# Performance work log

Hardware: AMD Instinct MI355X
Metric: run time of the kernel (lower is better)

## Reference

```python
import jax, jax.numpy as jnp
import numpy as np

BATCH, NSTEPS, IN_F, OUT_F = 8192, 16, 256, 512


def setup_inputs() -> dict:
    key = jax.random.key(0)
    ks = jax.random.split(key, 20)
    r = jax.random.normal
    return {
        "x": r(ks[0], (BATCH, NSTEPS, IN_F), jnp.float32),
        "C": r(ks[1], (BATCH, OUT_F, 1), jnp.float32),
        "H": r(ks[2], (BATCH, OUT_F, 1), jnp.float32),
        "fg_w_c": r(ks[3], (OUT_F, 1), jnp.float32),
        "fg_w_h": r(ks[4], (OUT_F, OUT_F), jnp.float32),
        "fg_w_x": r(ks[5], (OUT_F, IN_F), jnp.float32),
        "fg_b": r(ks[6], (OUT_F, 1), jnp.float32),
        "ig_w_c": r(ks[7], (OUT_F, 1), jnp.float32),
        "ig_w_h": r(ks[8], (OUT_F, OUT_F), jnp.float32),
        "ig_w_x": r(ks[9], (OUT_F, IN_F), jnp.float32),
        "ig_b": r(ks[10], (OUT_F, 1), jnp.float32),
        "in_w_h": r(ks[11], (OUT_F, OUT_F), jnp.float32),
        "in_w_x": r(ks[12], (OUT_F, IN_F), jnp.float32),
        "in_b": r(ks[13], (OUT_F, 1), jnp.float32),
        "og_w_cn": r(ks[14], (OUT_F, 1), jnp.float32),
        "og_w_h": r(ks[15], (OUT_F, OUT_F), jnp.float32),
        "og_w_x": r(ks[16], (OUT_F, IN_F), jnp.float32),
        "og_b": r(ks[17], (OUT_F, 1), jnp.float32),
        "n": 3,
    }


def reference(x, C, H,
              fg_w_c, fg_w_h, fg_w_x, fg_b,
              ig_w_c, ig_w_h, ig_w_x, ig_b,
              in_w_h, in_w_x, in_b,
              og_w_cn, og_w_h, og_w_x, og_b,
              n):
    # x: [B, T, IN] -> current step [B, IN, 1]
    x_cur = x[:, n, :, None]
    # peephole LSTM gates; matmul broadcasts [O,O] @ [B,O,1] -> [B,O,1]
    fg = jax.nn.sigmoid(fg_w_c * C + jnp.matmul(fg_w_h, H) + jnp.matmul(fg_w_x, x_cur) + fg_b)
    ig = jax.nn.sigmoid(ig_w_c * C + jnp.matmul(ig_w_h, H) + jnp.matmul(ig_w_x, x_cur) + ig_b)
    inn = jnp.tanh(jnp.matmul(in_w_h, H) + jnp.matmul(in_w_x, x_cur) + in_b)
    cm = fg * C + ig * inn
    og = jax.nn.sigmoid(og_w_cn * cm + jnp.matmul(og_w_h, H) + jnp.matmul(og_w_x, x_cur) + og_b)
    h = og * jnp.tanh(cm)
    return (cm, h)
```

## Files before the change

kernel.cpp:

```cpp
#include <hip/hip_runtime.h>


typedef _Float16 half8 __attribute__((ext_vector_type(8)));
typedef _Float16 half4v __attribute__((ext_vector_type(4)));
typedef float floatx4 __attribute__((ext_vector_type(4)));

#define BATCH 8192
#define NSTEPS 16
#define IN_F 256
#define OUT_F 512
#define KDIM 768
#define NDIM 2048
#define HSIZE ((size_t)BATCH * OUT_F)

#define BM 128
#define BN 128
#define BK 64

__device__ __forceinline__ void async_copy16(const void* gptr, void* lptr) {
  __builtin_amdgcn_global_load_lds(
      (const __attribute__((address_space(1))) unsigned int*)gptr,
      (__attribute__((address_space(3))) unsigned int*)lptr,
      16, 0, 0);
}

__device__ __forceinline__ float sigmoidf_(float x) {
  return 1.0f / (1.0f + __expf(-x));
}

__device__ __forceinline__ float tanhf_(float x) {
  x = fminf(fmaxf(x, -20.0f), 20.0f);
  float e = __expf(2.0f * x);
  return (e - 1.0f) / (e + 1.0f);
}

__global__ void pack_A(const float* __restrict__ H, const float* __restrict__ x,
                       const int* __restrict__ nptr, _Float16* __restrict__ A) {
  const int n = *nptr;
  const int b = blockIdx.x;
  const int k = threadIdx.x * 4;
  float4 v;
  if (k < OUT_F)
    v = *(const float4*)(H + (size_t)b * OUT_F + k);
  else
    v = *(const float4*)(x + ((size_t)b * NSTEPS + n) * IN_F + (k - OUT_F));
  half4v h = {(_Float16)v.x, (_Float16)v.y, (_Float16)v.z, (_Float16)v.w};
  *(half4v*)(A + (size_t)b * KDIM + k) = h;
}

__global__ void pack_W(const float* __restrict__ fg_w_h, const float* __restrict__ fg_w_x,
                       const float* __restrict__ ig_w_h, const float* __restrict__ ig_w_x,
                       const float* __restrict__ in_w_h, const float* __restrict__ in_w_x,
                       const float* __restrict__ og_w_h, const float* __restrict__ og_w_x,
                       _Float16* __restrict__ W) {
  const int row = blockIdx.x;
  const int g  = (row >> 4) & 3;
  const int jj = ((row >> 6) << 4) | (row & 15);
  const int k = threadIdx.x * 4;
  const float* src;
  if (k < OUT_F) {
    const float* wh = (g == 0) ? fg_w_h : (g == 1) ? ig_w_h : (g == 2) ? in_w_h : og_w_h;
    src = wh + (size_t)jj * OUT_F + k;
  } else {
    const float* wx = (g == 0) ? fg_w_x : (g == 1) ? ig_w_x : (g == 2) ? in_w_x : og_w_x;
    src = wx + (size_t)jj * IN_F + (k - OUT_F);
  }
  float4 v = *(const float4*)src;
  half4v h = {(_Float16)v.x, (_Float16)v.y, (_Float16)v.z, (_Float16)v.w};
  *(half4v*)(W + (size_t)row * KDIM + k) = h;
}

__global__ __launch_bounds__(256) void gemm_lstm(
    const _Float16* __restrict__ A, const _Float16* __restrict__ W,
    const float* __restrict__ C,
    const float* __restrict__ fg_w_c, const float* __restrict__ fg_b,
    const float* __restrict__ ig_w_c, const float* __restrict__ ig_b,
    const float* __restrict__ in_b,
    const float* __restrict__ og_w_cn, const float* __restrict__ og_b,
    float* __restrict__ out) {
  __shared__ __align__(16) _Float16 As[BM * BK];
  __shared__ __align__(16) _Float16 Bs[BN * BK];

  const int tid = threadIdx.x;
  const int lane = tid & 63;
  const int wave = tid >> 6;
  const int quad = lane >> 4;
  const int l16 = lane & 15;
  const int m0 = blockIdx.y * BM;
  const int n0 = blockIdx.x * BN;
  const int mw = (wave >> 1) * 64;
  const int nw = (wave & 1) * 64;

  const int jj = (((n0 + nw) >> 6) << 4) | l16;
  const float fwc = fg_w_c[jj], fb = fg_b[jj];
  const float iwc = ig_w_c[jj], ib = ig_b[jj];
  const float nb  = in_b[jj];
  const float owc = og_w_cn[jj], ob = og_b[jj];

  floatx4 acc[4][4] = {};

  for (int kt = 0; kt < KDIM; kt += BK) {
    __syncthreads();
#pragma unroll
    for (int r = 0; r < 4; ++r) {
      const int g = r * 256 + tid;
      const int row = g >> 3;
      const int cl = g & 7;
      const int cg = cl ^ (row & 7);
      async_copy16(A + (size_t)(m0 + row) * KDIM + kt + cg * 8,
                   (_Float16*)As + g * 8);
      async_copy16(W + (size_t)(n0 + row) * KDIM + kt + cg * 8,
                   (_Float16*)Bs + g * 8);
    }
    __syncthreads();

#pragma unroll
    for (int ks = 0; ks < 2; ++ks) {
      half8 af[4], bf[4];
#pragma unroll
      for (int i = 0; i < 4; ++i) {
        const int row = mw + i * 16 + l16;
        const int chunk = ks * 4 + quad;
        const int gran = row * 8 + (chunk ^ (row & 7));
        af[i] = *(const half8*)(As + gran * 8);
      }
#pragma unroll
      for (int j = 0; j < 4; ++j) {
        const int row = nw + j * 16 + l16;
        const int chunk = ks * 4 + quad;
        const int gran = row * 8 + (chunk ^ (row & 7));
        bf[j] = *(const half8*)(Bs + gran * 8);
      }
#pragma unroll
      for (int i = 0; i < 4; ++i)
#pragma unroll
        for (int j = 0; j < 4; ++j)
          acc[i][j] = __builtin_amdgcn_mfma_f32_16x16x32_f16(af[i], bf[j], acc[i][j], 0, 0, 0);
    }
  }

#pragma unroll
  for (int i = 0; i < 4; ++i) {
    const int rbase = m0 + mw + i * 16 + quad * 4;
#pragma unroll
    for (int r = 0; r < 4; ++r) {
      const int b = rbase + r;
      const float c = C[(size_t)b * OUT_F + jj];
      const float fg  = sigmoidf_(fwc * c + acc[i][0][r] + fb);
      const float ig  = sigmoidf_(iwc * c + acc[i][1][r] + ib);
      const float inn = tanhf_(acc[i][2][r] + nb);
      const float cm  = fg * c + ig * inn;
      const float og  = sigmoidf_(owc * cm + acc[i][3][r] + ob);
      out[(size_t)b * OUT_F + jj] = cm;
      out[HSIZE + (size_t)b * OUT_F + jj] = og * tanhf_(cm);
    }
  }
}

extern "C" void kernel_launch(void* const* d_in, const int* in_sizes, int n_in,
                              void* d_out, int out_size, void* d_ws, size_t ws_size,
                              hipStream_t stream) {
  const float* x       = (const float*)d_in[0];
  const float* C       = (const float*)d_in[1];
  const float* H       = (const float*)d_in[2];
  const float* fg_w_c  = (const float*)d_in[3];
  const float* fg_w_h  = (const float*)d_in[4];
  const float* fg_w_x  = (const float*)d_in[5];
  const float* fg_b    = (const float*)d_in[6];
  const float* ig_w_c  = (const float*)d_in[7];
  const float* ig_w_h  = (const float*)d_in[8];
  const float* ig_w_x  = (const float*)d_in[9];
  const float* ig_b    = (const float*)d_in[10];
  const float* in_w_h  = (const float*)d_in[11];
  const float* in_w_x  = (const float*)d_in[12];
  const float* in_b    = (const float*)d_in[13];
  const float* og_w_cn = (const float*)d_in[14];
  const float* og_w_h  = (const float*)d_in[15];
  const float* og_w_x  = (const float*)d_in[16];
  const float* og_b    = (const float*)d_in[17];
  const int*   nptr    = (const int*)d_in[18];

  char* ws = (char*)d_ws;
  _Float16* Apk = (_Float16*)ws;
  _Float16* Wpk = (_Float16*)(ws + 12582912);
  (void)ws_size; (void)in_sizes; (void)n_in; (void)out_size;

  pack_A<<<BATCH, 192, 0, stream>>>(H, x, nptr, Apk);
  pack_W<<<NDIM, 192, 0, stream>>>(fg_w_h, fg_w_x, ig_w_h, ig_w_x,
                                   in_w_h, in_w_x, og_w_h, og_w_x, Wpk);
  dim3 grid(NDIM / BN, BATCH / BM);
  gemm_lstm<<<grid, 256, 0, stream>>>(Apk, Wpk, C,
                                      fg_w_c, fg_b, ig_w_c, ig_b, in_b,
                                      og_w_cn, og_b, (float*)d_out);
}
```

Before: 264.8 us.

## Merge pack kernels, raise GEMM occupancy hint, hoist C loads in epilogue

Combines the A and W packing kernels into one launch to remove a kernel launch and its tail. Adds a min-blocks-per-SM hint of 4 to the GEMM so the compiler limits registers for higher occupancy. The epilogue now loads all C values and computes tanh of the input gate before the main loop, so the loads can be issued together. The occupancy hint may force register spills given the 64 accumulator floats plus the extra epilogue arrays.

```diff
diff --git a/kernel.cpp b/kernel.cpp
--- a/kernel.cpp
+++ b/kernel.cpp
@@ -34,43 +34,45 @@
   return (e - 1.0f) / (e + 1.0f);
 }
 
-__global__ void pack_A(const float* __restrict__ H, const float* __restrict__ x,
-                       const int* __restrict__ nptr, _Float16* __restrict__ A) {
-  const int n = *nptr;
-  const int b = blockIdx.x;
-  const int k = threadIdx.x * 4;
-  float4 v;
-  if (k < OUT_F)
-    v = *(const float4*)(H + (size_t)b * OUT_F + k);
-  else
-    v = *(const float4*)(x + ((size_t)b * NSTEPS + n) * IN_F + (k - OUT_F));
-  half4v h = {(_Float16)v.x, (_Float16)v.y, (_Float16)v.z, (_Float16)v.w};
-  *(half4v*)(A + (size_t)b * KDIM + k) = h;
-}
-
-__global__ void pack_W(const float* __restrict__ fg_w_h, const float* __restrict__ fg_w_x,
-                       const float* __restrict__ ig_w_h, const float* __restrict__ ig_w_x,
-                       const float* __restrict__ in_w_h, const float* __restrict__ in_w_x,
-                       const float* __restrict__ og_w_h, const float* __restrict__ og_w_x,
-                       _Float16* __restrict__ W) {
-  const int row = blockIdx.x;
-  const int g  = (row >> 4) & 3;
-  const int jj = ((row >> 6) << 4) | (row & 15);
+__global__ void pack_AW(const float* __restrict__ H, const float* __restrict__ x,
+                        const int* __restrict__ nptr,
+                        const float* __restrict__ fg_w_h, const float* __restrict__ fg_w_x,
+                        const float* __restrict__ ig_w_h, const float* __restrict__ ig_w_x,
+                        const float* __restrict__ in_w_h, const float* __restrict__ in_w_x,
+                        const float* __restrict__ og_w_h, const float* __restrict__ og_w_x,
+                        _Float16* __restrict__ A, _Float16* __restrict__ W) {
+  const int blk = blockIdx.x;
   const int k = threadIdx.x * 4;
   const float* src;
-  if (k < OUT_F) {
-    const float* wh = (g == 0) ? fg_w_h : (g == 1) ? ig_w_h : (g == 2) ? in_w_h : og_w_h;
-    src = wh + (size_t)jj * OUT_F + k;
+  _Float16* dst;
+  if (blk < BATCH) {
+    const int b = blk;
+    if (k < OUT_F) {
+      src = H + (size_t)b * OUT_F + k;
+    } else {
+      const int n = *nptr;
+      src = x + ((size_t)b * NSTEPS + n) * IN_F + (k - OUT_F);
+    }
+    dst = A + (size_t)b * KDIM + k;
   } else {
-    const float* wx = (g == 0) ? fg_w_x : (g == 1) ? ig_w_x : (g == 2) ? in_w_x : og_w_x;
-    src = wx + (size_t)jj * IN_F + (k - OUT_F);
+    const int row = blk - BATCH;
+    const int g  = (row >> 4) & 3;
+    const int jj = ((row >> 6) << 4) | (row & 15);
+    if (k < OUT_F) {
+      const float* wh = (g == 0) ? fg_w_h : (g == 1) ? ig_w_h : (g == 2) ? in_w_h : og_w_h;
+      src = wh + (size_t)jj * OUT_F + k;
+    } else {
+      const float* wx = (g == 0) ? fg_w_x : (g == 1) ? ig_w_x : (g == 2) ? in_w_x : og_w_x;
+      src = wx + (size_t)jj * IN_F + (k - OUT_F);
+    }
+    dst = W + (size_t)row * KDIM + k;
   }
   float4 v = *(const float4*)src;
   half4v h = {(_Float16)v.x, (_Float16)v.y, (_Float16)v.z, (_Float16)v.w};
-  *(half4v*)(W + (size_t)row * KDIM + k) = h;
-}
-
-__global__ __launch_bounds__(256) void gemm_lstm(
+  *(half4v*)dst = h;
+}
+
+__global__ __launch_bounds__(256, 4) void gemm_lstm(
     const _Float16* __restrict__ A, const _Float16* __restrict__ W,
     const float* __restrict__ C,
     const float* __restrict__ fg_w_c, const float* __restrict__ fg_b,
@@ -139,17 +141,30 @@
     }
   }
 
+  float cv[16];
 #pragma unroll
   for (int i = 0; i < 4; ++i) {
     const int rbase = m0 + mw + i * 16 + quad * 4;
 #pragma unroll
+    for (int r = 0; r < 4; ++r)
+      cv[i * 4 + r] = C[(size_t)(rbase + r) * OUT_F + jj];
+  }
+  float inn[16];
+#pragma unroll
+  for (int i = 0; i < 4; ++i)
+#pragma unroll
+    for (int r = 0; r < 4; ++r)
+      inn[i * 4 + r] = tanhf_(acc[i][2][r] + nb);
+#pragma unroll
+  for (int i = 0; i < 4; ++i) {
+    const int rbase = m0 + mw + i * 16 + quad * 4;
+#pragma unroll
     for (int r = 0; r < 4; ++r) {
       const int b = rbase + r;
-      const float c = C[(size_t)b * OUT_F + jj];
+      const float c = cv[i * 4 + r];
       const float fg  = sigmoidf_(fwc * c + acc[i][0][r] + fb);
       const float ig  = sigmoidf_(iwc * c + acc[i][1][r] + ib);
-      const float inn = tanhf_(acc[i][2][r] + nb);
-      const float cm  = fg * c + ig * inn;
+      const float cm  = fg * c + ig * inn[i * 4 + r];
       const float og  = sigmoidf_(owc * cm + acc[i][3][r] + ob);
       out[(size_t)b * OUT_F + jj] = cm;
       out[HSIZE + (size_t)b * OUT_F + jj] = og * tanhf_(cm);
@@ -185,9 +200,10 @@
   _Float16* Wpk = (_Float16*)(ws + 12582912);
   (void)ws_size; (void)in_sizes; (void)n_in; (void)out_size;
 
-  pack_A<<<BATCH, 192, 0, stream>>>(H, x, nptr, Apk);
-  pack_W<<<NDIM, 192, 0, stream>>>(fg_w_h, fg_w_x, ig_w_h, ig_w_x,
-                                   in_w_h, in_w_x, og_w_h, og_w_x, Wpk);
+  pack_AW<<<BATCH + NDIM, 192, 0, stream>>>(H, x, nptr,
+                                            fg_w_h, fg_w_x, ig_w_h, ig_w_x,
+                                            in_w_h, in_w_x, og_w_h, og_w_x,
+                                            Apk, Wpk);
   dim3 grid(NDIM / BN, BATCH / BM);
   gemm_lstm<<<grid, 256, 0, stream>>>(Apk, Wpk, C,
                                       fg_w_c, fg_b, ig_w_c, ig_b, in_b,
```

New measurement: 259.2 us. -2.1%, faster.
